# Kernel tuning notes

Hardware: AMD Instinct MI355X
Metric: run time of the kernel (lower is better)

The kernel has to match this reference:

```python
import jax, jax.numpy as jnp
import numpy as np

B, T, D = 2, 4096, 512
H, W = 8, 32
HD = D // H            # 64
HIDDEN = 3 * D         # SwiGLU expansion = 3
SCALE = float(np.sqrt(HD))
EPS = 1e-5


def setup_inputs() -> dict:
    key = jax.random.key(0)
    ks = jax.random.split(key, 8)
    s = 0.02  # small init for weight matrices
    return {
        "x": jax.random.normal(ks[0], (B, T, D), dtype=jnp.float32),
        "pre_g": jnp.ones((D,), jnp.float32), "pre_b": jnp.zeros((D,), jnp.float32),
        "wq": jax.random.normal(ks[1], (D, D), jnp.float32) * s,
        "wkv": jax.random.normal(ks[2], (D, 2 * D), jnp.float32) * s,
        "wo": jax.random.normal(ks[3], (D, D), jnp.float32) * s,
        "attn_g": jnp.ones((D,), jnp.float32), "attn_b": jnp.zeros((D,), jnp.float32),
        "freqs": jax.random.normal(ks[4], (D,), jnp.float32) * 0.02,
        "phases": jnp.zeros((D,), jnp.float32),
        "amp": jnp.full((1,), 0.1, jnp.float32),
        "w_gate": jax.random.normal(ks[5], (D, HIDDEN), jnp.float32) * s,
        "w_val": jax.random.normal(ks[6], (D, HIDDEN), jnp.float32) * s,
        "w_proj": jax.random.normal(ks[7], (HIDDEN, D), jnp.float32) * s,
        "ffn_g": jnp.ones((D,), jnp.float32), "ffn_b": jnp.zeros((D,), jnp.float32),
    }


def _ln(x, g, b):
    mu = jnp.mean(x, axis=-1, keepdims=True)
    var = jnp.mean(jnp.square(x - mu), axis=-1, keepdims=True)
    return (x - mu) * jax.lax.rsqrt(var + EPS) * g + b


def _gather_window(z):
    # z: (B, T, H, C) -> nb: (B, T, W, H, C) with nb[:, t, w] = z[:, t-1-w] (zeros if t-1-w < 0)
    zp = jnp.pad(z, ((0, 0), (W, 0), (0, 0), (0, 0)))
    idx = jnp.arange(T)[:, None] + (W - 1) - jnp.arange(W)[None, :]  # (T, W), values in [0, T+W-1)
    return zp[:, idx]  # (B, T, W, H, C)


def reference(x, pre_g, pre_b, wq, wkv, wo, attn_g, attn_b,
              freqs, phases, amp, w_gate, w_val, w_proj, ffn_g, ffn_b):
    h = _ln(x, pre_g, pre_b)

    # ---- multi-head causal tension (sigmoid local attention) ----
    q = (h @ wq).reshape(B, T, H, HD)
    kv = (h @ wkv).reshape(B, T, H, 2 * HD)
    nb_kv = _gather_window(kv)                     # (B, T, W, H, 2*HD)
    nb_k, nb_v = nb_kv[..., :HD], nb_kv[..., HD:]
    tau = jax.nn.sigmoid(jnp.einsum('bthd,btwhd->bthw', q, nb_k) / SCALE)
    msg = jnp.einsum('bthw,btwhd->bthd', tau, nb_v).reshape(B, T, D)
    h = _ln(h + msg @ wo, attn_g, attn_b)

    # ---- oscillatory modulation ----
    pos = jnp.arange(T, dtype=jnp.float32)[:, None]  # (T, 1)
    mod = jnp.sin(pos * freqs + phases)              # (T, D)
    y = h * (1.0 + amp * mod)[None]

    # ---- SwiGLU FFN ----
    z = (jax.nn.silu(y @ w_gate) * (y @ w_val)) @ w_proj
    return _ln(y + z, ffn_g, ffn_b)
```

## Files before the change

### kernel.cpp

```cpp
#include <hip/hip_runtime.h>
#include <hip/hip_bf16.h>
#include <math.h>

#define T_LEN   4096
#define D_DIM   512
#define H_NUM   8
#define HD_DIM  64
#define W_WIN   32
#define HID_DIM 1536
#define M_ROWS  8192
#define QKV_LD  1536

typedef __hip_bfloat16 bf16;
typedef __bf16  bf16x8 __attribute__((ext_vector_type(8)));
typedef float   f32x4  __attribute__((ext_vector_type(4)));

__device__ __forceinline__ float b2f(bf16 x) { return __bfloat162float(x); }
__device__ __forceinline__ bf16  f2b(float x){ return __float2bfloat16(x); }

__device__ __forceinline__ float rdP(const void* p, int i, bool f32) {
  return f32 ? ((const float*)p)[i] : b2f(((const bf16*)p)[i]);
}

__device__ __forceinline__ float wave_reduce_sum(float v) {
  #pragma unroll
  for (int off = 32; off; off >>= 1) v += __shfl_xor(v, off, 64);
  return v;
}

__device__ __forceinline__ bool detect_f32(const unsigned* __restrict__ x) {
  int lane = threadIdx.x & 63;
  int votes = 0;
  #pragma unroll
  for (int i = 0; i < 4; ++i) {
    unsigned e = (x[lane * 4 + i] >> 7) & 0xffu;
    votes += (e >= 90u && e <= 140u) ? 1 : 0;
  }
  float v = wave_reduce_sum((float)votes);
  return v < 200.f;
}

__device__ __forceinline__ void gload_lds16(const bf16* g, bf16* l) {
  __builtin_amdgcn_global_load_lds(
      (const __attribute__((address_space(1))) unsigned int*)g,
      (__attribute__((address_space(3))) unsigned int*)l, 16, 0, 0);
}

__device__ __forceinline__ void swizzle_xy(int gx, int& bx, int& by) {
  int lid = blockIdx.x;
  int sub = lid & 7;
  int grp = lid >> 3;
  bx = grp % gx;
  by = (grp / gx) * 8 + sub;
}

__global__ __launch_bounds__(256) void ln_kernel(
    const void* __restrict__ in, const void* __restrict__ g, const void* __restrict__ bb,
    void* __restrict__ out, int mode,
    const void* __restrict__ freqs, const void* __restrict__ phases,
    const void* __restrict__ amp,
    const unsigned* __restrict__ xdet, int in_follows, int out_follows)
{
  bool f32  = detect_f32(xdet);
  bool inF  = f32 && (in_follows != 0);
  bool outF = f32 && (out_follows != 0);

  int wave = threadIdx.x >> 6;
  int lane = threadIdx.x & 63;
  int row  = blockIdx.x * 4 + wave;

  float x[8];
  if (inF) {
    const float* rp = (const float*)in + (size_t)row * D_DIM + lane * 8;
    float4 v0 = *reinterpret_cast<const float4*>(rp);
    float4 v1 = *reinterpret_cast<const float4*>(rp + 4);
    x[0]=v0.x; x[1]=v0.y; x[2]=v0.z; x[3]=v0.w;
    x[4]=v1.x; x[5]=v1.y; x[6]=v1.z; x[7]=v1.w;
  } else {
    bf16x8 v = *reinterpret_cast<const bf16x8*>(
        (const bf16*)in + (size_t)row * D_DIM + lane * 8);
    #pragma unroll
    for (int i = 0; i < 8; ++i) x[i] = (float)v[i];
  }

  float s = 0.f, s2 = 0.f;
  #pragma unroll
  for (int i = 0; i < 8; ++i) { s += x[i]; s2 += x[i]*x[i]; }
  s  = wave_reduce_sum(s);
  s2 = wave_reduce_sum(s2);
  float mu   = s * (1.f / D_DIM);
  float var  = s2 * (1.f / D_DIM) - mu * mu;
  float rstd = rsqrtf(var + 1e-5f);

  int t = row & (T_LEN - 1);
  float ampf = (mode == 1) ? rdP(amp, 0, f32) : 0.f;

  float o[8];
  #pragma unroll
  for (int i = 0; i < 8; ++i) {
    int d = lane * 8 + i;
    float val = (x[i] - mu) * rstd * rdP(g, d, f32) + rdP(bb, d, f32);
    if (mode == 1) {
      float m = sinf(fmaf((float)t, rdP(freqs, d, f32), rdP(phases, d, f32)));
      val *= (1.f + ampf * m);
    }
    o[i] = val;
  }

  if (outF) {
    float* op = (float*)out + (size_t)row * D_DIM + lane * 8;
    *reinterpret_cast<float4*>(op)     = make_float4(o[0], o[1], o[2], o[3]);
    *reinterpret_cast<float4*>(op + 4) = make_float4(o[4], o[5], o[6], o[7]);
  } else {
    bf16x8 ov;
    #pragma unroll
    for (int i = 0; i < 8; ++i) ov[i] = (__bf16)o[i];
    *reinterpret_cast<bf16x8*>((bf16*)out + (size_t)row * D_DIM + lane * 8) = ov;
  }
}

__global__ __launch_bounds__(256) void transpose_all_kernel(
    const void* s0, const void* s1, const void* s2, const void* s3,
    const void* s4, const void* s5,
    bf16* d0, bf16* d1, bf16* d2, bf16* d3, bf16* d4, bf16* d5,
    const unsigned* __restrict__ xdet)
{
  bool f32 = detect_f32(xdet);
  int bid = blockIdx.x;
  const void* src; bf16* dst; int R, C, lid, tiles_x;
  if      (bid < 256)  { src=s0; dst=d0; R=512;  C=512;  lid=bid;      tiles_x=16; }
  else if (bid < 768)  { src=s1; dst=d1; R=512;  C=1024; lid=bid-256;  tiles_x=32; }
  else if (bid < 1024) { src=s2; dst=d2; R=512;  C=512;  lid=bid-768;  tiles_x=16; }
  else if (bid < 1792) { src=s3; dst=d3; R=512;  C=1536; lid=bid-1024; tiles_x=48; }
  else if (bid < 2560) { src=s4; dst=d4; R=512;  C=1536; lid=bid-1792; tiles_x=48; }
  else                 { src=s5; dst=d5; R=1536; C=512;  lid=bid-2560; tiles_x=16; }

  __shared__ bf16 tile[32][33];
  int tx = threadIdx.x & 31;
  int ty = threadIdx.x >> 5;
  int c0 = (lid % tiles_x) * 32;
  int r0 = (lid / tiles_x) * 32;
  #pragma unroll
  for (int j = 0; j < 32; j += 8)
    tile[ty + j][tx] = f2b(rdP(src, (size_t)(r0 + ty + j) * C + c0 + tx, f32));
  __syncthreads();
  #pragma unroll
  for (int j = 0; j < 32; j += 8)
    dst[(size_t)(c0 + ty + j) * R + r0 + tx] = tile[tx][ty + j];
}

#define BK 64
__global__ __launch_bounds__(256) void gemm64_kernel(
    const bf16* __restrict__ A, const bf16* __restrict__ Bt,
    bf16* Cout, const bf16* extra, int N, int K, int lda, int mode, int gx)
{
  __shared__ alignas(16) bf16 As[64 * BK];
  __shared__ alignas(16) bf16 Bs[64 * BK];

  int bx, by; swizzle_xy(gx, bx, by);
  int lane = threadIdx.x & 63;
  int wid  = threadIdx.x >> 6;
  int quad = lane >> 4;
  int l16  = lane & 15;
  int mbase = by * 64;
  int nbase = bx * 64;
  int wm = (wid >> 1) * 32;
  int wn = (wid & 1) * 32;

  int srow   = wid * 16 + (lane >> 3);
  int schunk = (lane & 7) ^ (lane >> 3);
  const bf16* Ag = A  + (size_t)(mbase + srow) * lda + schunk * 8;
  const bf16* Bg = Bt + (size_t)(nbase + srow) * K   + schunk * 8;

  f32x4 acc[2][2] = {};

  for (int kit = K / BK; kit > 0; --kit) {
    __syncthreads();
    #pragma unroll
    for (int it = 0; it < 2; ++it) {
      gload_lds16(Ag + (size_t)(it * 8) * lda, &As[(wid * 16 + it * 8) * BK]);
      gload_lds16(Bg + (size_t)(it * 8) * K,   &Bs[(wid * 16 + it * 8) * BK]);
    }
    Ag += BK; Bg += BK;
    __syncthreads();

    #pragma unroll
    for (int ko = 0; ko < 2; ++ko) {
      bf16x8 a[2], b[2];
      #pragma unroll
      for (int i = 0; i < 2; ++i) {
        int c = (ko * 4 + quad) ^ (l16 & 7);
        a[i] = *reinterpret_cast<const bf16x8*>(&As[(wm + i * 16 + l16) * BK + c * 8]);
        b[i] = *reinterpret_cast<const bf16x8*>(&Bs[(wn + i * 16 + l16) * BK + c * 8]);
      }
      #pragma unroll
      for (int i = 0; i < 2; ++i)
        #pragma unroll
        for (int j = 0; j < 2; ++j)
          acc[i][j] = __builtin_amdgcn_mfma_f32_16x16x32_bf16(a[i], b[j], acc[i][j], 0, 0, 0);
    }
  }

  #pragma unroll
  for (int i = 0; i < 2; ++i) {
    #pragma unroll
    for (int j = 0; j < 2; ++j) {
      #pragma unroll
      for (int r = 0; r < 4; ++r) {
        int row = mbase + wm + i * 16 + quad * 4 + r;
        int col = nbase + wn + j * 16 + l16;
        size_t idx = (size_t)row * N + col;
        float c = acc[i][j][r];
        if (mode == 1) c += b2f(extra[idx]);
        Cout[idx] = f2b(c);
      }
    }
  }
}

__global__ __launch_bounds__(256) void gemm_gateval_kernel(
    const bf16* __restrict__ A, const bf16* __restrict__ Btg,
    const bf16* __restrict__ Btv, bf16* __restrict__ Cout,
    int N, int K, int lda, int gx)
{
  __shared__ alignas(16) bf16 As [64 * BK];
  __shared__ alignas(16) bf16 Bgs[64 * BK];
  __shared__ alignas(16) bf16 Bvs[64 * BK];

  int bx, by; swizzle_xy(gx, bx, by);
  int lane = threadIdx.x & 63;
  int wid  = threadIdx.x >> 6;
  int quad = lane >> 4;
  int l16  = lane & 15;
  int mbase = by * 64;
  int nbase = bx * 64;
  int wm = (wid >> 1) * 32;
  int wn = (wid & 1) * 32;

  int srow   = wid * 16 + (lane >> 3);
  int schunk = (lane & 7) ^ (lane >> 3);
  const bf16* Ag  = A   + (size_t)(mbase + srow) * lda + schunk * 8;
  const bf16* Bgg = Btg + (size_t)(nbase + srow) * K   + schunk * 8;
  const bf16* Bvg = Btv + (size_t)(nbase + srow) * K   + schunk * 8;

  f32x4 accg[2][2] = {};
  f32x4 accv[2][2] = {};

  for (int kit = K / BK; kit > 0; --kit) {
    __syncthreads();
    #pragma unroll
    for (int it = 0; it < 2; ++it) {
      gload_lds16(Ag  + (size_t)(it * 8) * lda, &As [(wid * 16 + it * 8) * BK]);
      gload_lds16(Bgg + (size_t)(it * 8) * K,   &Bgs[(wid * 16 + it * 8) * BK]);
      gload_lds16(Bvg + (size_t)(it * 8) * K,   &Bvs[(wid * 16 + it * 8) * BK]);
    }
    Ag += BK; Bgg += BK; Bvg += BK;
    __syncthreads();

    #pragma unroll
    for (int ko = 0; ko < 2; ++ko) {
      bf16x8 a[2], bg[2], bv[2];
      #pragma unroll
      for (int i = 0; i < 2; ++i) {
        int c = (ko * 4 + quad) ^ (l16 & 7);
        a[i]  = *reinterpret_cast<const bf16x8*>(&As [(wm + i * 16 + l16) * BK + c * 8]);
        bg[i] = *reinterpret_cast<const bf16x8*>(&Bgs[(wn + i * 16 + l16) * BK + c * 8]);
        bv[i] = *reinterpret_cast<const bf16x8*>(&Bvs[(wn + i * 16 + l16) * BK + c * 8]);
      }
      #pragma unroll
      for (int i = 0; i < 2; ++i)
        #pragma unroll
        for (int j = 0; j < 2; ++j) {
          accg[i][j] = __builtin_amdgcn_mfma_f32_16x16x32_bf16(a[i], bg[j], accg[i][j], 0, 0, 0);
          accv[i][j] = __builtin_amdgcn_mfma_f32_16x16x32_bf16(a[i], bv[j], accv[i][j], 0, 0, 0);
        }
    }
  }

  #pragma unroll
  for (int i = 0; i < 2; ++i) {
    #pragma unroll
    for (int j = 0; j < 2; ++j) {
      #pragma unroll
      for (int r = 0; r < 4; ++r) {
        int row = mbase + wm + i * 16 + quad * 4 + r;
        int col = nbase + wn + j * 16 + l16;
        float g = accg[i][j][r];
        float v = accv[i][j][r];
        Cout[(size_t)row * N + col] = f2b(g / (1.f + expf(-g)) * v);
      }
    }
  }
}

#define VT_BYTES 9216
#define PL_BYTES 2304
__device__ __forceinline__ int vt_addr(int d, int t) {
  return d * 144 + t * 2;
}

__global__ __launch_bounds__(256) void attn_mfma_kernel(bf16* qkv)
{
  __shared__ alignas(16) char lds_raw[4 * (VT_BYTES + PL_BYTES)];
  int lane = threadIdx.x & 63;
  int widx = threadIdx.x >> 6;
  int u    = blockIdx.x * 4 + widx;
  int tile = u >> 3, head = u & 7;
  int rowbase = tile * 16;
  int t0   = rowbase & (T_LEN - 1);
  int l16  = lane & 15, quad = lane >> 4;

  char* wbase = lds_raw + widx * (VT_BYTES + PL_BYTES);
  char* Vl = wbase;
  bf16* Pl = (bf16*)(wbase + VT_BYTES);

  {
    #pragma unroll
    for (int it = 0; it < 6; ++it) {
      int chunk = it * 64 + lane;
      int t  = chunk >> 3;
      int dc = chunk & 7;
      int row = rowbase - 32 + t;
      if (row < 0) row = 0;
      bf16x8 v = *reinterpret_cast<const bf16x8*>(
          qkv + (size_t)row * QKV_LD + 512 + head * 128 + 64 + dc * 8);
      #pragma unroll
      for (int jj = 0; jj < 8; ++jj)
        *(bf16*)(Vl + vt_addr(dc * 8 + jj, t)) = (bf16)(__bf16)v[jj];
    }
    bf16x8 z = {};
    *reinterpret_cast<bf16x8*>(Vl + vt_addr(lane, 48)) = z;
    *reinterpret_cast<bf16x8*>(Vl + vt_addr(lane, 56)) = z;
  }

  bf16x8 aq0, aq1;
  {
    const bf16* qrow = qkv + (size_t)(rowbase + l16) * QKV_LD + head * HD_DIM + quad * 8;
    aq0 = *reinterpret_cast<const bf16x8*>(qrow);
    aq1 = *reinterpret_cast<const bf16x8*>(qrow + 32);
  }

  f32x4 sacc[3] = {};
  #pragma unroll
  for (int jt = 0; jt < 3; ++jt) {
    int tok = rowbase - 32 + jt * 16 + l16;
    if (tok < 0) tok = 0;
    const bf16* krow = qkv + (size_t)tok * QKV_LD + 512 + head * 128 + quad * 8;
    bf16x8 b0 = *reinterpret_cast<const bf16x8*>(krow);
    bf16x8 b1 = *reinterpret_cast<const bf16x8*>(krow + 32);
    sacc[jt] = __builtin_amdgcn_mfma_f32_16x16x32_bf16(aq0, b0, sacc[jt], 0, 0, 0);
    sacc[jt] = __builtin_amdgcn_mfma_f32_16x16x32_bf16(aq1, b1, sacc[jt], 0, 0, 0);
  }

  #pragma unroll
  for (int jt = 0; jt < 3; ++jt) {
    int j = jt * 16 + l16;
    #pragma unroll
    for (int r = 0; r < 4; ++r) {
      int i = quad * 4 + r;
      bool valid = (j >= i) && (j <= i + 31) && (t0 - 32 + j >= 0);
      float tau = valid ? 1.f / (1.f + expf(-sacc[jt][r] * 0.125f)) : 0.f;
      Pl[i * 72 + j] = f2b(tau);
    }
  }
  {
    #pragma unroll
    for (int r = 0; r < 4; ++r) Pl[(quad * 4 + r) * 72 + 48 + l16] = f2b(0.f);
  }

  __syncthreads();

  bf16x8 ap0 = *reinterpret_cast<const bf16x8*>((char*)Pl + l16 * 144 + quad * 16);
  bf16x8 ap1 = *reinterpret_cast<const bf16x8*>((char*)Pl + l16 * 144 + 64 + quad * 16);

  f32x4 macc[4] = {};
  #pragma unroll
  for (int nt = 0; nt < 4; ++nt) {
    int d = nt * 16 + l16;
    bf16x8 bv0 = *reinterpret_cast<const bf16x8*>(Vl + vt_addr(d, quad * 8));
    bf16x8 bv1 = *reinterpret_cast<const bf16x8*>(Vl + vt_addr(d, 32 + quad * 8));
    macc[nt] = __builtin_amdgcn_mfma_f32_16x16x32_bf16(ap0, bv0, macc[nt], 0, 0, 0);
    macc[nt] = __builtin_amdgcn_mfma_f32_16x16x32_bf16(ap1, bv1, macc[nt], 0, 0, 0);
  }

  #pragma unroll
  for (int nt = 0; nt < 4; ++nt)
    #pragma unroll
    for (int r = 0; r < 4; ++r)
      qkv[(size_t)(rowbase + quad * 4 + r) * QKV_LD + head * HD_DIM + nt * 16 + l16] =
          f2b(macc[nt][r]);
}

extern "C" void kernel_launch(void* const* d_in, const int* in_sizes, int n_in,
                              void* d_out, int out_size, void* d_ws, size_t ws_size,
                              hipStream_t stream)
{
  const void* x      = d_in[0];
  const void* pre_g  = d_in[1];
  const void* pre_b  = d_in[2];
  const void* wq     = d_in[3];
  const void* wkv    = d_in[4];
  const void* wo     = d_in[5];
  const void* attn_g = d_in[6];
  const void* attn_b = d_in[7];
  const void* freqs  = d_in[8];
  const void* phases = d_in[9];
  const void* amp    = d_in[10];
  const void* w_gate = d_in[11];
  const void* w_val  = d_in[12];
  const void* w_proj = d_in[13];
  const void* ffn_g  = d_in[14];
  const void* ffn_b  = d_in[15];
  const unsigned* xdet = (const unsigned*)x;

  char* ws = (char*)d_ws;
  bf16* Btqkv = (bf16*)(ws + 512);
  bf16* Bto   = (bf16*)(ws + 1573376);
  bf16* Btg   = (bf16*)(ws + 2097664);
  bf16* Btv   = (bf16*)(ws + 3670528);
  bf16* Btp   = (bf16*)(ws + 5243392);
  bf16* h     = (bf16*)(ws + 6816256);
  bf16* qkvb  = (bf16*)(ws + 15204864);
  bf16* gb    = qkvb;

  transpose_all_kernel<<<3328, 256, 0, stream>>>(
      wq, wkv, wo, w_gate, w_val, w_proj,
      Btqkv, Btqkv + 512 * 512, Bto, Btg, Btv, Btp, xdet);

  ln_kernel<<<2048, 256, 0, stream>>>(x, pre_g, pre_b, h, 0,
                                      nullptr, nullptr, nullptr, xdet, 1, 0);

  gemm64_kernel<<<3072, 256, 0, stream>>>(h, Btqkv, qkvb, nullptr, 1536, 512, 512, 0, 24);

  attn_mfma_kernel<<<1024, 256, 0, stream>>>(qkvb);

  gemm64_kernel<<<1024, 256, 0, stream>>>(qkvb, Bto, h, h, 512, 512, QKV_LD, 1, 8);

  ln_kernel<<<2048, 256, 0, stream>>>(h, attn_g, attn_b, h, 1,
                                      freqs, phases, amp, xdet, 0, 0);

  gemm_gateval_kernel<<<3072, 256, 0, stream>>>(h, Btg, Btv, gb, 1536, 512, 512, 24);

  gemm64_kernel<<<1024, 256, 0, stream>>>(gb, Btp, h, h, 512, 1536, QKV_LD, 1, 8);

  ln_kernel<<<2048, 256, 0, stream>>>(h, ffn_g, ffn_b, d_out, 0,
                                      nullptr, nullptr, nullptr, xdet, 0, 1);
}
```

Baseline: 289.4 us.

## Fuse all stages into one persistent cooperative kernel with grid syncs

Replaces nine separate kernel launches with a single cooperative persistent kernel. Blocks loop over work units for each stage and use grid.sync between stages, so per-launch overhead and inter-kernel gaps go away. The grid is capped at 1024 blocks, attention now runs two waves at a time within shared LDS, and the launch falls back to the old multi-kernel path if cooperative launch fails. The risks are grid-sync cost, lower per-stage parallelism, and halved attention concurrency per block.

```diff
diff --git a/kernel.cpp b/kernel.cpp
--- a/kernel.cpp
+++ b/kernel.cpp
@@ -1,6 +1,9 @@
 #include <hip/hip_runtime.h>
 #include <hip/hip_bf16.h>
+#include <hip/hip_cooperative_groups.h>
 #include <math.h>
+
+namespace cg = cooperative_groups;
 
 #define T_LEN   4096
 #define D_DIM   512
@@ -10,6 +13,7 @@
 #define HID_DIM 1536
 #define M_ROWS  8192
 #define QKV_LD  1536
+#define BK 64
 
 typedef __hip_bfloat16 bf16;
 typedef __bf16  bf16x8 __attribute__((ext_vector_type(8)));
@@ -46,29 +50,19 @@
       (__attribute__((address_space(3))) unsigned int*)l, 16, 0, 0);
 }
 
-__device__ __forceinline__ void swizzle_xy(int gx, int& bx, int& by) {
-  int lid = blockIdx.x;
-  int sub = lid & 7;
-  int grp = lid >> 3;
-  bx = grp % gx;
-  by = (grp / gx) * 8 + sub;
-}
-
-__global__ __launch_bounds__(256) void ln_kernel(
-    const void* __restrict__ in, const void* __restrict__ g, const void* __restrict__ bb,
-    void* __restrict__ out, int mode,
-    const void* __restrict__ freqs, const void* __restrict__ phases,
-    const void* __restrict__ amp,
-    const unsigned* __restrict__ xdet, int in_follows, int out_follows)
-{
-  bool f32  = detect_f32(xdet);
-  bool inF  = f32 && (in_follows != 0);
-  bool outF = f32 && (out_follows != 0);
-
-  int wave = threadIdx.x >> 6;
+struct Params {
+  const void *x, *pre_g, *pre_b, *wq, *wkv, *wo, *attn_g, *attn_b,
+             *freqs, *phases, *amp, *w_gate, *w_val, *w_proj, *ffn_g, *ffn_b;
+  void* out;
+  bf16 *Btqkv, *Bto, *Btg, *Btv, *Btp, *h, *qkvb;
+};
+
+__device__ __forceinline__ void ln_row(
+    const void* in, const void* g, const void* bb, void* out, int mode,
+    const void* freqs, const void* phases, const void* amp,
+    bool f32, bool inF, bool outF, int row)
+{
   int lane = threadIdx.x & 63;
-  int row  = blockIdx.x * 4 + wave;
-
   float x[8];
   if (inF) {
     const float* rp = (const float*)in + (size_t)row * D_DIM + lane * 8;
@@ -82,7 +76,6 @@
     #pragma unroll
     for (int i = 0; i < 8; ++i) x[i] = (float)v[i];
   }
-
   float s = 0.f, s2 = 0.f;
   #pragma unroll
   for (int i = 0; i < 8; ++i) { s += x[i]; s2 += x[i]*x[i]; }
@@ -106,7 +99,6 @@
     }
     o[i] = val;
   }
-
   if (outF) {
     float* op = (float*)out + (size_t)row * D_DIM + lane * 8;
     *reinterpret_cast<float4*>(op)     = make_float4(o[0], o[1], o[2], o[3]);
@@ -119,27 +111,23 @@
   }
 }
 
-__global__ __launch_bounds__(256) void transpose_all_kernel(
-    const void* s0, const void* s1, const void* s2, const void* s3,
-    const void* s4, const void* s5,
-    bf16* d0, bf16* d1, bf16* d2, bf16* d3, bf16* d4, bf16* d5,
-    const unsigned* __restrict__ xdet)
-{
-  bool f32 = detect_f32(xdet);
-  int bid = blockIdx.x;
+__device__ __forceinline__ void transpose_unit(const Params& p, bool f32,
+                                               int bid, char* smem)
+{
   const void* src; bf16* dst; int R, C, lid, tiles_x;
-  if      (bid < 256)  { src=s0; dst=d0; R=512;  C=512;  lid=bid;      tiles_x=16; }
-  else if (bid < 768)  { src=s1; dst=d1; R=512;  C=1024; lid=bid-256;  tiles_x=32; }
-  else if (bid < 1024) { src=s2; dst=d2; R=512;  C=512;  lid=bid-768;  tiles_x=16; }
-  else if (bid < 1792) { src=s3; dst=d3; R=512;  C=1536; lid=bid-1024; tiles_x=48; }
-  else if (bid < 2560) { src=s4; dst=d4; R=512;  C=1536; lid=bid-1792; tiles_x=48; }
-  else                 { src=s5; dst=d5; R=1536; C=512;  lid=bid-2560; tiles_x=16; }
-
-  __shared__ bf16 tile[32][33];
+  if      (bid < 256)  { src=p.wq;     dst=p.Btqkv;           R=512;  C=512;  lid=bid;      tiles_x=16; }
+  else if (bid < 768)  { src=p.wkv;    dst=p.Btqkv + 512*512; R=512;  C=1024; lid=bid-256;  tiles_x=32; }
+  else if (bid < 1024) { src=p.wo;     dst=p.Bto;             R=512;  C=512;  lid=bid-768;  tiles_x=16; }
+  else if (bid < 1792) { src=p.w_gate; dst=p.Btg;             R=512;  C=1536; lid=bid-1024; tiles_x=48; }
+  else if (bid < 2560) { src=p.w_val;  dst=p.Btv;             R=512;  C=1536; lid=bid-1792; tiles_x=48; }
+  else                 { src=p.w_proj; dst=p.Btp;             R=1536; C=512;  lid=bid-2560; tiles_x=16; }
+
+  bf16 (*tile)[33] = (bf16 (*)[33])smem;
   int tx = threadIdx.x & 31;
   int ty = threadIdx.x >> 5;
   int c0 = (lid % tiles_x) * 32;
   int r0 = (lid / tiles_x) * 32;
+  __syncthreads();
   #pragma unroll
   for (int j = 0; j < 32; j += 8)
     tile[ty + j][tx] = f2b(rdP(src, (size_t)(r0 + ty + j) * C + c0 + tx, f32));
@@ -149,23 +137,17 @@
     dst[(size_t)(c0 + ty + j) * R + r0 + tx] = tile[tx][ty + j];
 }
 
-#define BK 64
-__global__ __launch_bounds__(256) void gemm64_kernel(
+__device__ __forceinline__ void gemm64_tile(
     const bf16* __restrict__ A, const bf16* __restrict__ Bt,
-    bf16* Cout, const bf16* extra, int N, int K, int lda, int mode, int gx)
-{
-  __shared__ alignas(16) bf16 As[64 * BK];
-  __shared__ alignas(16) bf16 Bs[64 * BK];
-
-  int bx, by; swizzle_xy(gx, bx, by);
+    bf16* Cout, const bf16* extra, int N, int K, int lda, int mode,
+    int mbase, int nbase, char* smem)
+{
+  bf16* As = (bf16*)smem;
+  bf16* Bs = (bf16*)(smem + 8192);
   int lane = threadIdx.x & 63;
   int wid  = threadIdx.x >> 6;
-  int quad = lane >> 4;
-  int l16  = lane & 15;
-  int mbase = by * 64;
-  int nbase = bx * 64;
-  int wm = (wid >> 1) * 32;
-  int wn = (wid & 1) * 32;
+  int quad = lane >> 4, l16 = lane & 15;
+  int wm = (wid >> 1) * 32, wn = (wid & 1) * 32;
 
   int srow   = wid * 16 + (lane >> 3);
   int schunk = (lane & 7) ^ (lane >> 3);
@@ -202,9 +184,9 @@
   }
 
   #pragma unroll
-  for (int i = 0; i < 2; ++i) {
-    #pragma unroll
-    for (int j = 0; j < 2; ++j) {
+  for (int i = 0; i < 2; ++i)
+    #pragma unroll
+    for (int j = 0; j < 2; ++j)
       #pragma unroll
       for (int r = 0; r < 4; ++r) {
         int row = mbase + wm + i * 16 + quad * 4 + r;
@@ -214,28 +196,20 @@
         if (mode == 1) c += b2f(extra[idx]);
         Cout[idx] = f2b(c);
       }
-    }
-  }
-}
-
-__global__ __launch_bounds__(256) void gemm_gateval_kernel(
+}
+
+__device__ __forceinline__ void gateval_tile(
     const bf16* __restrict__ A, const bf16* __restrict__ Btg,
     const bf16* __restrict__ Btv, bf16* __restrict__ Cout,
-    int N, int K, int lda, int gx)
-{
-  __shared__ alignas(16) bf16 As [64 * BK];
-  __shared__ alignas(16) bf16 Bgs[64 * BK];
-  __shared__ alignas(16) bf16 Bvs[64 * BK];
-
-  int bx, by; swizzle_xy(gx, bx, by);
+    int N, int K, int lda, int mbase, int nbase, char* smem)
+{
+  bf16* As  = (bf16*)smem;
+  bf16* Bgs = (bf16*)(smem + 8192);
+  bf16* Bvs = (bf16*)(smem + 16384);
   int lane = threadIdx.x & 63;
   int wid  = threadIdx.x >> 6;
-  int quad = lane >> 4;
-  int l16  = lane & 15;
-  int mbase = by * 64;
-  int nbase = bx * 64;
-  int wm = (wid >> 1) * 32;
-  int wn = (wid & 1) * 32;
+  int quad = lane >> 4, l16 = lane & 15;
+  int wm = (wid >> 1) * 32, wn = (wid & 1) * 32;
 
   int srow   = wid * 16 + (lane >> 3);
   int schunk = (lane & 7) ^ (lane >> 3);
@@ -278,9 +252,9 @@
   }
 
   #pragma unroll
-  for (int i = 0; i < 2; ++i) {
-    #pragma unroll
-    for (int j = 0; j < 2; ++j) {
+  for (int i = 0; i < 2; ++i)
+    #pragma unroll
+    for (int j = 0; j < 2; ++j)
       #pragma unroll
       for (int r = 0; r < 4; ++r) {
         int row = mbase + wm + i * 16 + quad * 4 + r;
@@ -289,49 +263,39 @@
         float v = accv[i][j][r];
         Cout[(size_t)row * N + col] = f2b(g / (1.f + expf(-g)) * v);
       }
-    }
-  }
 }
 
 #define VT_BYTES 9216
 #define PL_BYTES 2304
-__device__ __forceinline__ int vt_addr(int d, int t) {
-  return d * 144 + t * 2;
-}
-
-__global__ __launch_bounds__(256) void attn_mfma_kernel(bf16* qkv)
-{
-  __shared__ alignas(16) char lds_raw[4 * (VT_BYTES + PL_BYTES)];
+#define ATTN_SET (VT_BYTES + PL_BYTES)
+__device__ __forceinline__ int vt_addr(int d, int t) { return d * 144 + t * 2; }
+
+__device__ __forceinline__ void attn_unit(bf16* qkv, int unit, char* wbase)
+{
   int lane = threadIdx.x & 63;
-  int widx = threadIdx.x >> 6;
-  int u    = blockIdx.x * 4 + widx;
-  int tile = u >> 3, head = u & 7;
+  int tile = unit >> 3, head = unit & 7;
   int rowbase = tile * 16;
-  int t0   = rowbase & (T_LEN - 1);
-  int l16  = lane & 15, quad = lane >> 4;
-
-  char* wbase = lds_raw + widx * (VT_BYTES + PL_BYTES);
+  int t0 = rowbase & (T_LEN - 1);
+  int l16 = lane & 15, quad = lane >> 4;
   char* Vl = wbase;
   bf16* Pl = (bf16*)(wbase + VT_BYTES);
 
-  {
-    #pragma unroll
-    for (int it = 0; it < 6; ++it) {
-      int chunk = it * 64 + lane;
-      int t  = chunk >> 3;
-      int dc = chunk & 7;
-      int row = rowbase - 32 + t;
-      if (row < 0) row = 0;
-      bf16x8 v = *reinterpret_cast<const bf16x8*>(
-          qkv + (size_t)row * QKV_LD + 512 + head * 128 + 64 + dc * 8);
-      #pragma unroll
-      for (int jj = 0; jj < 8; ++jj)
-        *(bf16*)(Vl + vt_addr(dc * 8 + jj, t)) = (bf16)(__bf16)v[jj];
-    }
-    bf16x8 z = {};
-    *reinterpret_cast<bf16x8*>(Vl + vt_addr(lane, 48)) = z;
-    *reinterpret_cast<bf16x8*>(Vl + vt_addr(lane, 56)) = z;
-  }
+  #pragma unroll
+  for (int it = 0; it < 6; ++it) {
+    int chunk = it * 64 + lane;
+    int t  = chunk >> 3;
+    int dc = chunk & 7;
+    int row = rowbase - 32 + t;
+    if (row < 0) row = 0;
+    bf16x8 v = *reinterpret_cast<const bf16x8*>(
+        qkv + (size_t)row * QKV_LD + 512 + head * 128 + 64 + dc * 8);
+    #pragma unroll
+    for (int jj = 0; jj < 8; ++jj)
+      *(bf16*)(Vl + vt_addr(dc * 8 + jj, t)) = (bf16)(__bf16)v[jj];
+  }
+  bf16x8 z = {};
+  *reinterpret_cast<bf16x8*>(Vl + vt_addr(lane, 48)) = z;
+  *reinterpret_cast<bf16x8*>(Vl + vt_addr(lane, 56)) = z;
 
   bf16x8 aq0, aq1;
   {
@@ -363,12 +327,8 @@
       Pl[i * 72 + j] = f2b(tau);
     }
   }
-  {
-    #pragma unroll
-    for (int r = 0; r < 4; ++r) Pl[(quad * 4 + r) * 72 + 48 + l16] = f2b(0.f);
-  }
-
-  __syncthreads();
+  #pragma unroll
+  for (int r = 0; r < 4; ++r) Pl[(quad * 4 + r) * 72 + 48 + l16] = f2b(0.f);
 
   bf16x8 ap0 = *reinterpret_cast<const bf16x8*>((char*)Pl + l16 * 144 + quad * 16);
   bf16x8 ap1 = *reinterpret_cast<const bf16x8*>((char*)Pl + l16 * 144 + 64 + quad * 16);
@@ -391,58 +351,190 @@
           f2b(macc[nt][r]);
 }
 
+__global__ __launch_bounds__(256, 4) void mega_kernel(Params p)
+{
+  __shared__ alignas(16) char smem[24576];
+  cg::grid_group grid = cg::this_grid();
+  bool f32 = detect_f32((const unsigned*)p.x);
+  int wave = threadIdx.x >> 6;
+  int G = (int)gridDim.x;
+
+  for (int u = blockIdx.x; u < 5376; u += G) {
+    if (u < 3328) transpose_unit(p, f32, u, smem);
+    else          ln_row(p.x, p.pre_g, p.pre_b, p.h, 0, nullptr, nullptr, nullptr,
+                         f32, f32, false, (u - 3328) * 4 + wave);
+  }
+  grid.sync();
+
+  #pragma unroll 1
+  for (int t = blockIdx.x; t < 3072; t += G) {
+    int sub = t & 7, gg = t >> 3;
+    int bx = gg >> 4;
+    int by = (gg & 15) * 8 + sub;
+    gemm64_tile(p.h, p.Btqkv, p.qkvb, nullptr, 1536, 512, 512, 0,
+                by * 64, bx * 64, smem);
+  }
+  grid.sync();
+
+  #pragma unroll 1
+  for (int b = blockIdx.x; b < 1024; b += G) {
+    int u0 = b * 4;
+    #pragma unroll 1
+    for (int ph = 0; ph < 2; ++ph) {
+      bool active = (wave >> 1) == ph;
+      int unit = u0 + ph * 2 + (wave & 1);
+      char* wbase = smem + (wave & 1) * ATTN_SET;
+      __syncthreads();
+      if (active) attn_unit(p.qkvb, unit, wbase);
+    }
+    __syncthreads();
+  }
+  grid.sync();
+
+  #pragma unroll 1
+  for (int t = blockIdx.x; t < 1024; t += G) {
+    int sub = t & 7, gg = t >> 3;
+    int bx = gg >> 4;
+    int by = (gg & 15) * 8 + sub;
+    gemm64_tile(p.qkvb, p.Bto, p.h, p.h, 512, 512, QKV_LD, 1,
+                by * 64, bx * 64, smem);
+  }
+  grid.sync();
+
+  #pragma unroll 1
+  for (int u = blockIdx.x; u < 2048; u += G)
+    ln_row(p.h, p.attn_g, p.attn_b, p.h, 1, p.freqs, p.phases, p.amp,
+           f32, false, false, u * 4 + wave);
+  grid.sync();
+
+  #pragma unroll 1
+  for (int t = blockIdx.x; t < 3072; t += G) {
+    int sub = t & 7, gg = t >> 3;
+    int bx = gg >> 4;
+    int by = (gg & 15) * 8 + sub;
+    gateval_tile(p.h, p.Btg, p.Btv, p.qkvb, 1536, 512, 512,
+                 by * 64, bx * 64, smem);
+  }
+  grid.sync();
+
+  #pragma unroll 1
+  for (int t = blockIdx.x; t < 1024; t += G) {
+    int sub = t & 7, gg = t >> 3;
+    int bx = gg >> 4;
+    int by = (gg & 15) * 8 + sub;
+    gemm64_tile(p.qkvb, p.Btp, p.h, p.h, 512, 1536, QKV_LD, 1,
+                by * 64, bx * 64, smem);
+  }
+  grid.sync();
+
+  #pragma unroll 1
+  for (int u = blockIdx.x; u < 2048; u += G)
+    ln_row(p.h, p.ffn_g, p.ffn_b, p.out, 0, nullptr, nullptr, nullptr,
+           f32, false, f32, u * 4 + wave);
+}
+
+__device__ __forceinline__ void swizzle_xy(int gx, int& bx, int& by) {
+  int lid = blockIdx.x;
+  int sub = lid & 7;
+  int grp = lid >> 3;
+  bx = grp % gx;
+  by = (grp / gx) * 8 + sub;
+}
+
+__global__ __launch_bounds__(256) void fb_transpose_all(Params p) {
+  __shared__ alignas(16) char smem[2304];
+  bool f32 = detect_f32((const unsigned*)p.x);
+  transpose_unit(p, f32, blockIdx.x, smem);
+}
+
+__global__ __launch_bounds__(256) void fb_ln(
+    const void* in, const void* g, const void* bb, void* out, int mode,
+    const void* freqs, const void* phases, const void* amp,
+    const unsigned* xdet, int inFollows, int outFollows)
+{
+  bool f32 = detect_f32(xdet);
+  ln_row(in, g, bb, out, mode, freqs, phases, amp,
+         f32, f32 && inFollows, f32 && outFollows,
+         blockIdx.x * 4 + (threadIdx.x >> 6));
+}
+
+__global__ __launch_bounds__(256) void fb_gemm64(
+    const bf16* A, const bf16* Bt, bf16* Cout, const bf16* extra,
+    int N, int K, int lda, int mode, int gx)
+{
+  __shared__ alignas(16) char smem[16384];
+  int bx, by; swizzle_xy(gx, bx, by);
+  gemm64_tile(A, Bt, Cout, extra, N, K, lda, mode, by * 64, bx * 64, smem);
+}
+
+__global__ __launch_bounds__(256) void fb_gateval(
+    const bf16* A, const bf16* Btg, const bf16* Btv, bf16* Cout,
+    int N, int K, int lda, int gx)
+{
+  __shared__ alignas(16) char smem[24576];
+  int bx, by; swizzle_xy(gx, bx, by);
+  gateval_tile(A, Btg, Btv, Cout, N, K, lda, by * 64, bx * 64, smem);
+}
+
+__global__ __launch_bounds__(256) void fb_attn(bf16* qkv) {
+  __shared__ alignas(16) char smem[4 * ATTN_SET];
+  int wave = threadIdx.x >> 6;
+  attn_unit(qkv, blockIdx.x * 4 + wave, smem + wave * ATTN_SET);
+}
+
 extern "C" void kernel_launch(void* const* d_in, const int* in_sizes, int n_in,
                               void* d_out, int out_size, void* d_ws, size_t ws_size,
                               hipStream_t stream)
 {
-  const void* x      = d_in[0];
-  const void* pre_g  = d_in[1];
-  const void* pre_b  = d_in[2];
-  const void* wq     = d_in[3];
-  const void* wkv    = d_in[4];
-  const void* wo     = d_in[5];
-  const void* attn_g = d_in[6];
-  const void* attn_b = d_in[7];
-  const void* freqs  = d_in[8];
-  const void* phases = d_in[9];
-  const void* amp    = d_in[10];
-  const void* w_gate = d_in[11];
-  const void* w_val  = d_in[12];
-  const void* w_proj = d_in[13];
-  const void* ffn_g  = d_in[14];
-  const void* ffn_b  = d_in[15];
-  const unsigned* xdet = (const unsigned*)x;
-
   char* ws = (char*)d_ws;
-  bf16* Btqkv = (bf16*)(ws + 512);
-  bf16* Bto   = (bf16*)(ws + 1573376);
-  bf16* Btg   = (bf16*)(ws + 2097664);
-  bf16* Btv   = (bf16*)(ws + 3670528);
-  bf16* Btp   = (bf16*)(ws + 5243392);
-  bf16* h     = (bf16*)(ws + 6816256);
-  bf16* qkvb  = (bf16*)(ws + 15204864);
-  bf16* gb    = qkvb;
-
-  transpose_all_kernel<<<3328, 256, 0, stream>>>(
-      wq, wkv, wo, w_gate, w_val, w_proj,
-      Btqkv, Btqkv + 512 * 512, Bto, Btg, Btv, Btp, xdet);
-
-  ln_kernel<<<2048, 256, 0, stream>>>(x, pre_g, pre_b, h, 0,
-                                      nullptr, nullptr, nullptr, xdet, 1, 0);
-
-  gemm64_kernel<<<3072, 256, 0, stream>>>(h, Btqkv, qkvb, nullptr, 1536, 512, 512, 0, 24);
-
-  attn_mfma_kernel<<<1024, 256, 0, stream>>>(qkvb);
-
-  gemm64_kernel<<<1024, 256, 0, stream>>>(qkvb, Bto, h, h, 512, 512, QKV_LD, 1, 8);
-
-  ln_kernel<<<2048, 256, 0, stream>>>(h, attn_g, attn_b, h, 1,
-                                      freqs, phases, amp, xdet, 0, 0);
-
-  gemm_gateval_kernel<<<3072, 256, 0, stream>>>(h, Btg, Btv, gb, 1536, 512, 512, 24);
-
-  gemm64_kernel<<<1024, 256, 0, stream>>>(gb, Btp, h, h, 512, 1536, QKV_LD, 1, 8);
-
-  ln_kernel<<<2048, 256, 0, stream>>>(h, ffn_g, ffn_b, d_out, 0,
-                                      nullptr, nullptr, nullptr, xdet, 0, 1);
-}
+  Params p;
+  p.x      = d_in[0];  p.pre_g  = d_in[1];  p.pre_b  = d_in[2];
+  p.wq     = d_in[3];  p.wkv    = d_in[4];  p.wo     = d_in[5];
+  p.attn_g = d_in[6];  p.attn_b = d_in[7];  p.freqs  = d_in[8];
+  p.phases = d_in[9];  p.amp    = d_in[10]; p.w_gate = d_in[11];
+  p.w_val  = d_in[12]; p.w_proj = d_in[13]; p.ffn_g  = d_in[14];
+  p.ffn_b  = d_in[15];
+  p.out    = d_out;
+  p.Btqkv  = (bf16*)(ws + 512);
+  p.Bto    = (bf16*)(ws + 1573376);
+  p.Btg    = (bf16*)(ws + 2097664);
+  p.Btv    = (bf16*)(ws + 3670528);
+  p.Btp    = (bf16*)(ws + 5243392);
+  p.h      = (bf16*)(ws + 6816256);
+  p.qkvb   = (bf16*)(ws + 15204864);
+
+  int maxB = 0;
+  hipError_t occ = hipOccupancyMaxActiveBlocksPerMultiprocessor(
+      &maxB, (const void*)mega_kernel, 256, 0);
+  bool coop_ok = false;
+  if (occ == hipSuccess && maxB > 0) {
+    int gridb = maxB * 256;
+    if (gridb > 1024) gridb = 1024;
+    gridb &= ~7;
+    if (gridb >= 64) {
+      void* args[] = { &p };
+      hipError_t e = hipLaunchCooperativeKernel(
+          (const void*)mega_kernel, dim3(gridb), dim3(256), args, 0, stream);
+      coop_ok = (e == hipSuccess);
+    }
+  }
+  if (coop_ok) return;
+
+  const unsigned* xdet = (const unsigned*)p.x;
+  fb_transpose_all<<<3328, 256, 0, stream>>>(p);
+  fb_ln<<<2048, 256, 0, stream>>>(p.x, p.pre_g, p.pre_b, p.h, 0,
+                                  nullptr, nullptr, nullptr, xdet, 1, 0);
+  fb_gemm64<<<3072, 256, 0, stream>>>(p.h, p.Btqkv, p.qkvb, nullptr,
+                                      1536, 512, 512, 0, 24);
+  fb_attn<<<1024, 256, 0, stream>>>(p.qkvb);
+  fb_gemm64<<<1024, 256, 0, stream>>>(p.qkvb, p.Bto, p.h, p.h,
+                                      512, 512, QKV_LD, 1, 8);
+  fb_ln<<<2048, 256, 0, stream>>>(p.h, p.attn_g, p.attn_b, p.h, 1,
+                                  p.freqs, p.phases, p.amp, xdet, 0, 0);
+  fb_gateval<<<3072, 256, 0, stream>>>(p.h, p.Btg, p.Btv, p.qkvb,
+                                       1536, 512, 512, 24);
+  fb_gemm64<<<1024, 256, 0, stream>>>(p.qkvb, p.Btp, p.h, p.h,
+                                      512, 1536, QKV_LD, 1, 8);
+  fb_ln<<<2048, 256, 0, stream>>>(p.h, p.ffn_g, p.ffn_b, p.out, 0,
+                                  nullptr, nullptr, nullptr, xdet, 0, 1);
+}
```

Measured after the change: 736.2 us. 2.54x slower.
